# Optimization experiments

Hardware: AMD Instinct MI355X
Metric: run time of the kernel (lower is better)

Reference implementation:

```python
import jax, jax.numpy as jnp
from jax import lax
import numpy as np

GWS = (2, 7, 7)          # grid_window_size
NUM_HEADS = 4
DIM = 256
HEAD_DIM = DIM // NUM_HEADS
SCALE = HEAD_DIM ** -0.5


def _rel_index(ws):
    d, h, w = ws
    coords = np.stack(np.meshgrid(np.arange(d), np.arange(h), np.arange(w), indexing='ij')).reshape(3, -1)
    rel = (coords[:, :, None] - coords[:, None, :]).transpose(1, 2, 0)
    rel[:, :, 0] += d - 1
    rel[:, :, 1] += h - 1
    rel[:, :, 2] += w - 1
    rel[:, :, 0] *= (2 * h - 1) * (2 * w - 1)
    rel[:, :, 1] *= (2 * w - 1)
    return rel.sum(-1)

RPI = jnp.asarray(_rel_index(GWS))  # (98, 98) int, constant buffer


def _ln(x, w, b, eps=1e-5):
    m = x.mean(-1, keepdims=True)
    v = ((x - m) ** 2).mean(-1, keepdims=True)
    return (x - m) * lax.rsqrt(v + eps) * w + b


def _attention(x, qkv_w, proj_w, proj_b, bias_table):
    # x: (num_windows, N, C); qkv has no bias in the original (qkv_bias=False)
    Bw, N, C = x.shape
    qkv = (x @ qkv_w.T).reshape(Bw, N, 3, NUM_HEADS, HEAD_DIM).transpose(2, 0, 3, 1, 4)
    q, k, v = qkv[0] * SCALE, qkv[1], qkv[2]
    scores = jnp.einsum('bhnd,bhmd->bhnm', q, k)
    bias = bias_table[RPI.reshape(-1)].reshape(N, N, NUM_HEADS).transpose(2, 0, 1)
    a = jax.nn.softmax(scores + bias[None], axis=-1)
    out = jnp.einsum('bhnm,bhmd->bhnd', a, v).transpose(0, 2, 1, 3).reshape(Bw, N, C)
    return out @ proj_w.T + proj_b


def _window_partition(x):
    B, D, H, W, C = x.shape
    d, h, w = GWS
    x = x.reshape(B, D // d, d, H // h, h, W // w, w, C).transpose(0, 1, 3, 5, 2, 4, 6, 7)
    return x.reshape(-1, d * h * w, C)


def _window_reverse(win, B, D, H, W):
    d, h, w = GWS
    x = win.reshape(B, D // d, H // h, W // w, d, h, w, -1).transpose(0, 1, 4, 2, 5, 3, 6, 7)
    return x.reshape(B, D, H, W, -1)


def _grid_partition(x):
    B, D, H, W, C = x.shape
    d, h, w = GWS
    x = x.reshape(B, d, D // d, h, H // h, w, W // w, C).transpose(0, 2, 4, 6, 1, 3, 5, 7)
    return x.reshape(-1, d * h * w, C)


def _grid_reverse(g, B, D, H, W):
    d, h, w = GWS
    x = g.reshape(B, D // d, H // h, W // w, d, h, w, -1).transpose(0, 4, 1, 5, 2, 6, 3, 7)
    return x.reshape(B, D, H, W, -1)


def _conv3d(x, w, b):
    y = lax.conv_general_dilated(x, w, (1, 1, 1), 'SAME',
                                 dimension_numbers=('NCDHW', 'OIDHW', 'NCDHW'))
    return y + b[None, :, None, None, None]


def _leaky(x):
    return jnp.where(x >= 0, x, 0.01 * x)


def setup_inputs() -> dict:
    key = jax.random.key(0)
    ks = jax.random.split(key, 12)
    B, D, H, W = 2, 8, 56, 56
    dim = DIM
    TBL = (2 * GWS[0] - 1) * (2 * GWS[1] - 1) * (2 * GWS[2] - 1)  # 507
    p = lambda k, s: jax.random.normal(k, s, jnp.float32) * 0.02
    return {
        'input': jax.random.normal(ks[0], (B, dim, D, H, W), jnp.float32),
        'n1w': jnp.ones((dim,), jnp.float32), 'n1b': jnp.zeros((dim,), jnp.float32),
        'n2w': jnp.ones((dim,), jnp.float32), 'n2b': jnp.zeros((dim,), jnp.float32),
        'wqkv': p(ks[1], (3 * dim, dim)),
        'wprojw': p(ks[2], (dim, dim)), 'wprojb': jnp.zeros((dim,), jnp.float32),
        'wbias': p(ks[3], (TBL, NUM_HEADS)),
        'gqkv': p(ks[4], (3 * dim, dim)),
        'gprojw': p(ks[5], (dim, dim)), 'gprojb': jnp.zeros((dim,), jnp.float32),
        'gbias': p(ks[6], (TBL, NUM_HEADS)),
        'f1c1w': p(ks[7], (128, 128, 3, 3, 3)), 'f1c1b': jnp.zeros((128,), jnp.float32),
        'f1c2w': p(ks[8], (128, 128, 3, 3, 3)), 'f1c2b': jnp.zeros((128,), jnp.float32),
        'g1c1w': p(ks[9], (128, 128, 3, 3, 3)), 'g1c1b': jnp.zeros((128,), jnp.float32),
        'g1c2w': p(ks[10], (128, 128, 3, 3, 3)), 'g1c2b': jnp.zeros((128,), jnp.float32),
    }


def reference(input, n1w, n1b, n2w, n2b, wqkv, wprojw, wprojb, wbias,
              gqkv, gprojw, gprojb, gbias,
              f1c1w, f1c1b, f1c2w, f1c2b, g1c1w, g1c1b, g1c2w, g1c2b):
    B, C, D, H, W = input.shape
    x = input.transpose(0, 2, 3, 4, 1)  # b d h w c
    x = _ln(x, n1w, n1b)
    pd = (GWS[0] - D % GWS[0]) % GWS[0]
    ph = (GWS[1] - H % GWS[1]) % GWS[1]
    pw = (GWS[2] - W % GWS[2]) % GWS[2]
    if pd or ph or pw:
        x = jnp.pad(x, ((0, 0), (0, pd), (0, ph), (0, pw), (0, 0)))
    Dp, Hp, Wp = D + pd, H + ph, W + pw
    # block (window) attention
    win = _window_partition(x)
    win = _attention(win, wqkv, wprojw, wprojb, wbias)
    xw = _window_reverse(win, B, Dp, Hp, Wp)
    # grid attention
    y = _ln(xw, n2w, n2b)
    g = _grid_partition(y)
    g = _attention(g, gqkv, gprojw, gprojb, gbias)
    y = _grid_reverse(g, B, Dp, Hp, Wp) + xw
    if pd or ph or pw:
        y = y[:, :D, :H, :W, :]
    y = y.transpose(0, 4, 1, 2, 3)  # b c d h w
    s = input + y
    # reversible conv block: split 256 -> 128/128
    x1, x2 = s[:, :C // 2], s[:, C // 2:]
    y1 = x1 + _conv3d(_leaky(_conv3d(x2, f1c1w, f1c1b)), f1c2w, f1c2b)
    y2 = x2 + _conv3d(_leaky(_conv3d(y1, g1c1w, g1c1b)), g1c2w, g1c2b)
    return jnp.concatenate([y1, y2], axis=1)
```

## Files before the change

### kernel.cpp

```cpp
#include <hip/hip_runtime.h>
#include <stdint.h>


typedef unsigned short u16;
typedef __attribute__((ext_vector_type(8))) short short8;
typedef __attribute__((ext_vector_type(4))) float f32x4;

#define TOK   50176
#define CH    256
#define SPAT  25088
#define PLANE 3136

__device__ __forceinline__ float b2f(u16 u) {
    union { uint32_t i; float f; } v; v.i = ((uint32_t)u) << 16; return v.f;
}
__device__ __forceinline__ u16 f2b(float f) {
    union { float f; uint32_t i; } v; v.f = f;
    uint32_t i = v.i;
    uint32_t r = i + 0x7FFFu + ((i >> 16) & 1u);
    return (u16)(r >> 16);
}

__global__ __launch_bounds__(256) void ln1_kernel(
    const float* __restrict__ x, const float* __restrict__ w,
    const float* __restrict__ bsh, u16* __restrict__ out)
{
    int t = blockIdx.x * 256 + threadIdx.x;
    int b = t / SPAT, sp = t % SPAT;
    const float* px = x + (size_t)b * CH * SPAT + sp;
    float s = 0.f, ss = 0.f;
    for (int c = 0; c < CH; c++) { float v = px[(size_t)c * SPAT]; s += v; ss += v * v; }
    float mean = s * (1.0f / CH);
    float var  = ss * (1.0f / CH) - mean * mean;
    float rstd = rsqrtf(var + 1e-5f);
    u16* po = out + (size_t)t * CH;
    for (int c = 0; c < CH; c++) {
        float v = (px[(size_t)c * SPAT] - mean) * rstd * w[c] + bsh[c];
        po[c] = f2b(v);
    }
}

__global__ __launch_bounds__(256) void ln2_kernel(
    const u16* __restrict__ x, const float* __restrict__ w,
    const float* __restrict__ bsh, u16* __restrict__ out)
{
    int wave = threadIdx.x >> 6, lane = threadIdx.x & 63;
    int t = blockIdx.x * 4 + wave;
    const u16* px = x + (size_t)t * CH + lane * 4;
    ushort4 v4 = *(const ushort4*)px;
    float v0 = b2f(v4.x), v1 = b2f(v4.y), v2 = b2f(v4.z), v3 = b2f(v4.w);
    float s = v0 + v1 + v2 + v3;
    float ss = v0*v0 + v1*v1 + v2*v2 + v3*v3;
    for (int o = 32; o > 0; o >>= 1) {
        s  += __shfl_xor(s,  o, 64);
        ss += __shfl_xor(ss, o, 64);
    }
    float mean = s * (1.0f / CH);
    float rstd = rsqrtf(ss * (1.0f / CH) - mean * mean + 1e-5f);
    float4 w4 = *(const float4*)(w + lane * 4);
    float4 b4 = *(const float4*)(bsh + lane * 4);
    ushort4 o4;
    o4.x = f2b((v0 - mean) * rstd * w4.x + b4.x);
    o4.y = f2b((v1 - mean) * rstd * w4.y + b4.y);
    o4.z = f2b((v2 - mean) * rstd * w4.z + b4.z);
    o4.w = f2b((v3 - mean) * rstd * w4.w + b4.w);
    *(ushort4*)(out + (size_t)t * CH + lane * 4) = o4;
}

__global__ __launch_bounds__(256) void gemm_mfma_kernel(
    const u16* __restrict__ A, const float* __restrict__ B,
    const float* __restrict__ bias, const u16* __restrict__ res,
    u16* __restrict__ C, int Nout)
{
    __shared__ u16 sAg[128][72];
    __shared__ u16 sBg[128][72];
    int tid = threadIdx.x;
    int m0 = blockIdx.x * 128, n0g = blockIdx.y * 128;
    int lane = tid & 63, wv = tid >> 6;
    int quad = lane >> 4, l15 = lane & 15;
    int mw = (wv & 1) * 64, nw = (wv >> 1) * 64;

    f32x4 zz = {0.f, 0.f, 0.f, 0.f};
    f32x4 acc[4][4];
    #pragma unroll
    for (int i = 0; i < 4; i++)
        #pragma unroll
        for (int j = 0; j < 4; j++) acc[i][j] = zz;

    for (int kc = 0; kc < 256; kc += 64) {
        __syncthreads();
        #pragma unroll
        for (int i = 0; i < 4; i++) {
            int unit = tid + i * 256;
            int row = unit >> 3, k8 = (unit & 7) << 3;
            *(uint4*)&sAg[row][k8] = *(const uint4*)(A + (size_t)(m0 + row) * 256 + kc + k8);
        }
        #pragma unroll
        for (int i = 0; i < 8; i++) {
            int unit = tid + i * 256;
            int row = unit >> 4, k4 = (unit & 15) << 2;
            float4 v = *(const float4*)(B + (size_t)(n0g + row) * 256 + kc + k4);
            ushort4 p;
            p.x = f2b(v.x); p.y = f2b(v.y); p.z = f2b(v.z); p.w = f2b(v.w);
            *(ushort4*)&sBg[row][k4] = p;
        }
        __syncthreads();
        #pragma unroll
        for (int kk = 0; kk < 2; kk++) {
            short8 afr[4], bfr[4];
            #pragma unroll
            for (int mt = 0; mt < 4; mt++)
                afr[mt] = *(const short8*)&sAg[mw + mt*16 + l15][kk*32 + quad*8];
            #pragma unroll
            for (int nt = 0; nt < 4; nt++)
                bfr[nt] = *(const short8*)&sBg[nw + nt*16 + l15][kk*32 + quad*8];
            #pragma unroll
            for (int mt = 0; mt < 4; mt++)
                #pragma unroll
                for (int nt = 0; nt < 4; nt++)
                    acc[mt][nt] = __builtin_amdgcn_mfma_f32_16x16x32_bf16(
                        afr[mt], bfr[nt], acc[mt][nt], 0, 0, 0);
        }
    }

    #pragma unroll
    for (int nt = 0; nt < 4; nt++) {
        int n = n0g + nw + nt*16 + l15;
        float bv = bias ? bias[n] : 0.f;
        #pragma unroll
        for (int mt = 0; mt < 4; mt++) {
            int m = m0 + mw + mt*16 + quad*4;
            #pragma unroll
            for (int r = 0; r < 4; r++) {
                float v = acc[mt][nt][r] + bv;
                size_t off = (size_t)(m + r) * Nout + n;
                if (res) v += b2f(res[off]);
                C[off] = f2b(v);
            }
        }
    }
}

__global__ __launch_bounds__(256) void attn_mfma_kernel(
    const u16* __restrict__ qkv, const float* __restrict__ btab,
    u16* __restrict__ outp, int mode)
{
    __shared__ u16 sKV[8704];
    __shared__ u16 sS[112][136];
    __shared__ float sBias[507];
    __shared__ int sTok[112];
    __shared__ int sEnc[112];
    __shared__ float sInv[112];

    int g = blockIdx.x, head = blockIdx.y, tid = threadIdx.x;
    int b  = g >> 8;
    int gd = (g >> 6) & 3, gh = (g >> 3) & 7, gw = g & 7;

    int lane = tid & 63, wv = tid >> 6;
    int quad = lane >> 4, l15 = lane & 15;
    int mts[2] = {wv, wv + 4};

    if (tid < 112) {
        int t = tid;
        int i = t / 49, r = t % 49, j = r / 7, k = r % 7;
        sEnc[tid] = i * 169 + j * 13 + k;
        int tokv = 0;
        if (t < 98) {
            int d, h, w;
            if (mode == 0) { d = gd*2 + i; h = gh*7 + j; w = gw*7 + k; }
            else           { d = i*4 + gd; h = j*8 + gh; w = k*8 + gw; }
            tokv = ((b*8 + d)*56 + h)*56 + w;
        }
        sTok[tid] = tokv;
    }
    for (int idx = tid; idx < 507; idx += 256) sBias[idx] = btab[idx * 4 + head];
    __syncthreads();

    for (int idx = tid; idx < 112 * 8; idx += 256) {
        int row = idx >> 3, c8 = (idx & 7) << 3;
        uint4 v = {0u, 0u, 0u, 0u};
        if (row < 98)
            v = *(const uint4*)(qkv + (size_t)sTok[row] * 768 + 256 + head * 64 + c8);
        *(uint4*)&sKV[row * 72 + c8] = v;
    }
    __syncthreads();

    short8 qf[2][2];
    #pragma unroll
    for (int mi = 0; mi < 2; mi++) {
        int mt = mts[mi];
        #pragma unroll
        for (int ks = 0; ks < 2; ks++) {
            short8 v;
            #pragma unroll
            for (int j = 0; j < 8; j++) v[j] = 0;
            int row = mt * 16 + l15;
            if (mt < 7 && row < 98)
                v = *(const short8*)(qkv + (size_t)sTok[row] * 768 + head * 64 + ks * 32 + quad * 8);
            qf[mi][ks] = v;
        }
    }

    f32x4 zz = {0.f, 0.f, 0.f, 0.f};
    #pragma unroll
    for (int mi = 0; mi < 2; mi++) {
        int mt = mts[mi];
        if (mt >= 7) continue;
        for (int nt = 0; nt < 7; nt++) {
            f32x4 acc = zz;
            acc = __builtin_amdgcn_mfma_f32_16x16x32_bf16(
                qf[mi][0], *(const short8*)&sKV[(nt*16 + l15) * 72 + quad*8], acc, 0, 0, 0);
            acc = __builtin_amdgcn_mfma_f32_16x16x32_bf16(
                qf[mi][1], *(const short8*)&sKV[(nt*16 + l15) * 72 + 32 + quad*8], acc, 0, 0, 0);
            int n = nt * 16 + l15;
            int en = (n < 98) ? sEnc[n] : 0;
            #pragma unroll
            for (int r = 0; r < 4; r++) {
                int m = mt * 16 + quad * 4 + r;
                float v;
                if (n < 98) {
                    int em = sEnc[m < 98 ? m : 97];
                    v = acc[r] * 0.125f + sBias[em - en + 253];
                } else v = -1e30f;
                sS[m][n] = f2b(v);
            }
        }
    }
    __syncthreads();

    for (int idx = tid; idx < 64 * 30; idx += 256) {
        int c = idx / 30, t = 98 + idx % 30;
        sKV[c * 136 + t] = 0;
    }
    for (int idx = tid; idx < 98 * 8; idx += 256) {
        int tok = idx >> 3, c8 = (idx & 7) << 3;
        uint4 v = *(const uint4*)(qkv + (size_t)sTok[tok] * 768 + 512 + head * 64 + c8);
        const u16* pv = (const u16*)&v;
        #pragma unroll
        for (int j = 0; j < 8; j++) sKV[(c8 + j) * 136 + tok] = pv[j];
    }

    {
        int row = tid >> 1, half = tid & 1;
        if (row < 112) {
            #pragma unroll
            for (int j = 0; j < 8; j++) sS[row][112 + half * 8 + j] = 0;
        }
        if (row < 98) {
            int c0 = half * 49;
            float mx = -1e30f;
            for (int j = 0; j < 49; j++) mx = fmaxf(mx, b2f(sS[row][c0 + j]));
            mx = fmaxf(mx, __shfl_xor(mx, 1, 64));
            float sum = 0.f;
            for (int j = 0; j < 49; j++) {
                float e = __expf(b2f(sS[row][c0 + j]) - mx);
                sum += e;
                sS[row][c0 + j] = f2b(e);
            }
            sum += __shfl_xor(sum, 1, 64);
            if (half == 0) sInv[row] = 1.0f / sum;
        }
    }
    __syncthreads();

    f32x4 po[2][4];
    #pragma unroll
    for (int mi = 0; mi < 2; mi++)
        #pragma unroll
        for (int nt = 0; nt < 4; nt++) po[mi][nt] = zz;

    #pragma unroll
    for (int mi = 0; mi < 2; mi++) {
        int mt = mts[mi];
        if (mt >= 7) continue;
        for (int ks = 0; ks < 4; ks++) {
            short8 ap = *(const short8*)&sS[mt*16 + l15][ks*32 + quad*8];
            #pragma unroll
            for (int nt = 0; nt < 4; nt++) {
                short8 bv = *(const short8*)&sKV[(nt*16 + l15) * 136 + ks*32 + quad*8];
                po[mi][nt] = __builtin_amdgcn_mfma_f32_16x16x32_bf16(ap, bv, po[mi][nt], 0, 0, 0);
            }
        }
    }

    #pragma unroll
    for (int mi = 0; mi < 2; mi++) {
        int mt = mts[mi];
        if (mt >= 7) continue;
        #pragma unroll
        for (int r = 0; r < 4; r++) {
            int m = mt * 16 + quad * 4 + r;
            if (m >= 98) continue;
            float inv = sInv[m];
            u16* dst = outp + (size_t)sTok[m] * 256 + head * 64 + l15;
            #pragma unroll
            for (int nt = 0; nt < 4; nt++)
                dst[nt * 16] = f2b(po[mi][nt][r] * inv);
        }
    }
}

__global__ __launch_bounds__(256) void ssplit_cl_kernel(
    const float* __restrict__ inp, const u16* __restrict__ y,
    u16* __restrict__ s1, u16* __restrict__ s2)
{
    __shared__ float sT[64][65];
    int t0 = blockIdx.x * 64;
    int b = t0 / SPAT, sp0 = t0 % SPAT;
    int tid = threadIdx.x;
    for (int cg = 0; cg < 4; cg++) {
        __syncthreads();
        #pragma unroll
        for (int i = 0; i < 16; i++) {
            int unit = tid + i * 256;
            int cl = unit >> 6, spl = unit & 63;
            sT[spl][cl] = inp[((size_t)(b * 256 + cg * 64 + cl)) * SPAT + sp0 + spl];
        }
        __syncthreads();
        int spl = tid >> 2, c16 = (tid & 3) * 16;
        int tok = t0 + spl;
        const u16* yp = y + (size_t)tok * 256 + cg * 64 + c16;
        int cbase = cg * 64 + c16;
        u16* dst = (cbase < 128) ? (s1 + (size_t)tok * 128 + cbase)
                                 : (s2 + (size_t)tok * 128 + cbase - 128);
        #pragma unroll
        for (int j = 0; j < 16; j++) {
            float v = sT[spl][c16 + j] + b2f(yp[j]);
            dst[j] = f2b(v);
        }
    }
}

__global__ __launch_bounds__(256) void convw_kernel(
    const float* __restrict__ w, u16* __restrict__ o)
{
    int e = blockIdx.x * 256 + threadIdx.x;
    int k = e >> 14;
    int r = e & 16383;
    o[e] = f2b(w[(size_t)r * 27 + k]);
}

__global__ __launch_bounds__(256) void conv_mfma_kernel(
    const u16* __restrict__ in_cl,
    const u16* __restrict__ wt27,
    const float* __restrict__ bias,
    const u16* __restrict__ res_cl,
    u16* __restrict__ out_cl,
    float* __restrict__ out_f32,
    int oc_base, int leaky)
{
    __shared__ u16 sA[64][136];
    __shared__ u16 sB[128][136];
    __shared__ int sD[64], sHH[64], sWW[64];

    int tid = threadIdx.x;
    int t0 = blockIdx.x * 64;
    int b = t0 / SPAT, sp0 = t0 % SPAT;

    if (tid < 64) {
        int sp = sp0 + tid;
        int d = sp / PLANE, r = sp % PLANE;
        sD[tid] = d; sHH[tid] = r / 56; sWW[tid] = r % 56;
    }

    int lane = tid & 63, wv = tid >> 6;
    int quad = lane >> 4, l15 = lane & 15;
    int n0 = wv * 32;

    f32x4 zz = {0.f, 0.f, 0.f, 0.f};
    f32x4 acc[4][2];
    #pragma unroll
    for (int i = 0; i < 4; i++) { acc[i][0] = zz; acc[i][1] = zz; }

    __syncthreads();

    for (int ko = 0; ko < 27; ko++) {
        int kd = ko / 9 - 1, kh = (ko / 3) % 3 - 1, kw = ko % 3 - 1;
        __syncthreads();
        #pragma unroll
        for (int i = 0; i < 4; i++) {
            int unit = tid + i * 256;
            int m = unit >> 4, k8 = (unit & 15) << 3;
            int dd = sD[m] + kd, hh = sHH[m] + kh, ww = sWW[m] + kw;
            uint4 v = {0u, 0u, 0u, 0u};
            if ((unsigned)dd < 8u && (unsigned)hh < 56u && (unsigned)ww < 56u) {
                size_t sp = (size_t)(b * 8 + dd) * PLANE + hh * 56 + ww;
                v = *(const uint4*)(in_cl + sp * 128 + k8);
            }
            *(uint4*)&sA[m][k8] = v;
        }
        const u16* wp = wt27 + (size_t)ko * 16384;
        #pragma unroll
        for (int i = 0; i < 8; i++) {
            int unit = tid + i * 256;
            int oc = unit >> 4, k8 = (unit & 15) << 3;
            *(uint4*)&sB[oc][k8] = *(const uint4*)(wp + oc * 128 + k8);
        }
        __syncthreads();
        #pragma unroll
        for (int kk = 0; kk < 4; kk++) {
            short8 afr[4], bfr[2];
            #pragma unroll
            for (int mt = 0; mt < 4; mt++)
                afr[mt] = *(const short8*)&sA[mt*16 + l15][kk*32 + quad*8];
            #pragma unroll
            for (int nt = 0; nt < 2; nt++)
                bfr[nt] = *(const short8*)&sB[n0 + nt*16 + l15][kk*32 + quad*8];
            #pragma unroll
            for (int mt = 0; mt < 4; mt++)
                #pragma unroll
                for (int nt = 0; nt < 2; nt++)
                    acc[mt][nt] = __builtin_amdgcn_mfma_f32_16x16x32_bf16(
                        afr[mt], bfr[nt], acc[mt][nt], 0, 0, 0);
        }
    }

    #pragma unroll
    for (int nt = 0; nt < 2; nt++) {
        int oc = n0 + nt*16 + l15;
        float bv = bias[oc];
        #pragma unroll
        for (int mt = 0; mt < 4; mt++) {
            int m = mt*16 + quad*4;
            #pragma unroll
            for (int r = 0; r < 4; r++) {
                float v = acc[mt][nt][r] + bv;
                if (leaky) v = (v >= 0.f) ? v : 0.01f * v;
                if (res_cl) v += b2f(res_cl[(size_t)(t0 + m + r) * 128 + oc]);
                acc[mt][nt][r] = v;
            }
        }
    }

    if (out_cl) {
        #pragma unroll
        for (int mt = 0; mt < 4; mt++) {
            int m = mt*16 + quad*4;
            #pragma unroll
            for (int nt = 0; nt < 2; nt++) {
                int oc = n0 + nt*16 + l15;
                #pragma unroll
                for (int r = 0; r < 4; r++)
                    out_cl[(size_t)(t0 + m + r) * 128 + oc] = f2b(acc[mt][nt][r]);
            }
        }
    }

    if (out_f32) {
        __syncthreads();
        float* sT = (float*)&sB[0][0];
        #pragma unroll
        for (int mt = 0; mt < 4; mt++) {
            int m = mt*16 + quad*4;
            #pragma unroll
            for (int nt = 0; nt < 2; nt++) {
                int oc = n0 + nt*16 + l15;
                #pragma unroll
                for (int r = 0; r < 4; r++)
                    sT[oc * 65 + m + r] = acc[mt][nt][r];
            }
        }
        __syncthreads();
        int oc = tid >> 1, half = tid & 1;
        size_t obase = ((size_t)b * 256 + oc_base + oc) * SPAT + sp0 + half * 32;
        const float* row = &sT[oc * 65 + half * 32];
        for (int j = 0; j < 32; j++) out_f32[obase + j] = row[j];
    }
}

extern "C" void kernel_launch(void* const* d_in, const int* in_sizes, int n_in,
                              void* d_out, int out_size, void* d_ws, size_t ws_size,
                              hipStream_t stream)
{
    const float* input  = (const float*)d_in[0];
    const float* n1w    = (const float*)d_in[1];
    const float* n1b    = (const float*)d_in[2];
    const float* n2w    = (const float*)d_in[3];
    const float* n2b    = (const float*)d_in[4];
    const float* wqkv   = (const float*)d_in[5];
    const float* wprojw = (const float*)d_in[6];
    const float* wprojb = (const float*)d_in[7];
    const float* wbias  = (const float*)d_in[8];
    const float* gqkv   = (const float*)d_in[9];
    const float* gprojw = (const float*)d_in[10];
    const float* gprojb = (const float*)d_in[11];
    const float* gbias  = (const float*)d_in[12];
    const float* f1c1w  = (const float*)d_in[13];
    const float* f1c1b  = (const float*)d_in[14];
    const float* f1c2w  = (const float*)d_in[15];
    const float* f1c2b  = (const float*)d_in[16];
    const float* g1c1w  = (const float*)d_in[17];
    const float* g1c1b  = (const float*)d_in[18];
    const float* g1c2w  = (const float*)d_in[19];
    const float* g1c2b  = (const float*)d_in[20];

    char* ws = (char*)d_ws;
    u16* xln   = (u16*)(ws);
    u16* qkv   = (u16*)(ws + 25690112);
    u16* attnb = (u16*)(ws + 102760448);
    u16* xw    = (u16*)(ws + 128450560);
    u16* y  = xln;
    u16* s1   = qkv;
    u16* s2   = (u16*)(ws + 25690112 + 12845056);
    u16* tb   = (u16*)(ws + 25690112 + 25690112);
    u16* y1cl = (u16*)(ws + 25690112 + 38535168);
    u16* cw0  = (u16*)(ws + 25690112 + 51380224);
    u16* cw1  = cw0 + 442368;
    u16* cw2  = cw1 + 442368;
    u16* cw3  = cw2 + 442368;

    float* outp = (float*)d_out;

    ln1_kernel<<<196, 256, 0, stream>>>(input, n1w, n1b, xln);
    gemm_mfma_kernel<<<dim3(392, 6), 256, 0, stream>>>(xln, wqkv, nullptr, nullptr, qkv, 768);
    attn_mfma_kernel<<<dim3(512, 4), 256, 0, stream>>>(qkv, wbias, attnb, 0);
    gemm_mfma_kernel<<<dim3(392, 2), 256, 0, stream>>>(attnb, wprojw, wprojb, nullptr, xw, 256);
    ln2_kernel<<<12544, 256, 0, stream>>>(xw, n2w, n2b, xln);
    gemm_mfma_kernel<<<dim3(392, 6), 256, 0, stream>>>(xln, gqkv, nullptr, nullptr, qkv, 768);
    attn_mfma_kernel<<<dim3(512, 4), 256, 0, stream>>>(qkv, gbias, attnb, 1);
    gemm_mfma_kernel<<<dim3(392, 2), 256, 0, stream>>>(attnb, gprojw, gprojb, xw, y, 256);
    ssplit_cl_kernel<<<784, 256, 0, stream>>>(input, y, s1, s2);
    convw_kernel<<<1728, 256, 0, stream>>>(f1c1w, cw0);
    convw_kernel<<<1728, 256, 0, stream>>>(f1c2w, cw1);
    convw_kernel<<<1728, 256, 0, stream>>>(g1c1w, cw2);
    convw_kernel<<<1728, 256, 0, stream>>>(g1c2w, cw3);
    conv_mfma_kernel<<<784, 256, 0, stream>>>(s2, cw0, f1c1b, nullptr, tb, nullptr, 0, 1);
    conv_mfma_kernel<<<784, 256, 0, stream>>>(tb, cw1, f1c2b, s1, y1cl, outp, 0, 0);
    conv_mfma_kernel<<<784, 256, 0, stream>>>(y1cl, cw2, g1c1b, nullptr, tb, nullptr, 0, 1);
    conv_mfma_kernel<<<784, 256, 0, stream>>>(tb, cw3, g1c2b, s2, nullptr, outp, 128, 0);
}
```

Baseline: 961.8 us.

## Load conv MFMA fragments directly from global memory, drop LDS staging

The 3D conv kernel stops staging input and weight tiles through shared memory each of its 27 taps, so the per-tap barriers go away. Each wave now loads its A and B MFMA fragments straight from global memory, relying on cache reuse. Blocks shrink to 128 threads (2 waves), each computing a 64-output-channel slice with a 4x4 accumulator tile. LDS is allocated dynamically only for the fp32 transpose store, which now writes float4 values. The risk is redundant global and L2 traffic, because there is no longer explicit on-chip reuse of weights across waves, and the larger accumulator tile raises register pressure.

```diff
diff --git a/kernel.cpp b/kernel.cpp
--- a/kernel.cpp
+++ b/kernel.cpp
@@ -340,7 +340,8 @@
     o[e] = f2b(w[(size_t)r * 27 + k]);
 }
 
-__global__ __launch_bounds__(256) void conv_mfma_kernel(
+extern __shared__ float conv_smem[];
+__global__ __launch_bounds__(128, 3) void conv_mfma_kernel(
     const u16* __restrict__ in_cl,
     const u16* __restrict__ wt27,
     const float* __restrict__ bias,
@@ -349,75 +350,70 @@
     float* __restrict__ out_f32,
     int oc_base, int leaky)
 {
-    __shared__ u16 sA[64][136];
-    __shared__ u16 sB[128][136];
-    __shared__ int sD[64], sHH[64], sWW[64];
-
     int tid = threadIdx.x;
     int t0 = blockIdx.x * 64;
     int b = t0 / SPAT, sp0 = t0 % SPAT;
-
-    if (tid < 64) {
-        int sp = sp0 + tid;
-        int d = sp / PLANE, r = sp % PLANE;
-        sD[tid] = d; sHH[tid] = r / 56; sWW[tid] = r % 56;
-    }
-
     int lane = tid & 63, wv = tid >> 6;
     int quad = lane >> 4, l15 = lane & 15;
-    int n0 = wv * 32;
+    int nw = wv * 64;
+
+    int dm[4], hm[4], wm[4];
+    const u16* abase[4];
+    #pragma unroll
+    for (int mt = 0; mt < 4; mt++) {
+        int sp = sp0 + mt*16 + l15;
+        dm[mt] = sp / PLANE;
+        int r = sp % PLANE;
+        hm[mt] = r / 56; wm[mt] = r % 56;
+        abase[mt] = in_cl + ((size_t)b * SPAT + sp) * 128 + quad * 8;
+    }
+    int boff[4];
+    #pragma unroll
+    for (int nt = 0; nt < 4; nt++)
+        boff[nt] = (nw + nt*16 + l15) * 128 + quad * 8;
 
     f32x4 zz = {0.f, 0.f, 0.f, 0.f};
-    f32x4 acc[4][2];
-    #pragma unroll
-    for (int i = 0; i < 4; i++) { acc[i][0] = zz; acc[i][1] = zz; }
-
-    __syncthreads();
+    f32x4 acc[4][4];
+    #pragma unroll
+    for (int i = 0; i < 4; i++)
+        #pragma unroll
+        for (int j = 0; j < 4; j++) acc[i][j] = zz;
+
+    short8 z8;
+    #pragma unroll
+    for (int j = 0; j < 8; j++) z8[j] = 0;
 
     for (int ko = 0; ko < 27; ko++) {
         int kd = ko / 9 - 1, kh = (ko / 3) % 3 - 1, kw = ko % 3 - 1;
-        __syncthreads();
-        #pragma unroll
-        for (int i = 0; i < 4; i++) {
-            int unit = tid + i * 256;
-            int m = unit >> 4, k8 = (unit & 15) << 3;
-            int dd = sD[m] + kd, hh = sHH[m] + kh, ww = sWW[m] + kw;
-            uint4 v = {0u, 0u, 0u, 0u};
-            if ((unsigned)dd < 8u && (unsigned)hh < 56u && (unsigned)ww < 56u) {
-                size_t sp = (size_t)(b * 8 + dd) * PLANE + hh * 56 + ww;
-                v = *(const uint4*)(in_cl + sp * 128 + k8);
-            }
-            *(uint4*)&sA[m][k8] = v;
-        }
-        const u16* wp = wt27 + (size_t)ko * 16384;
-        #pragma unroll
-        for (int i = 0; i < 8; i++) {
-            int unit = tid + i * 256;
-            int oc = unit >> 4, k8 = (unit & 15) << 3;
-            *(uint4*)&sB[oc][k8] = *(const uint4*)(wp + oc * 128 + k8);
-        }
-        __syncthreads();
+        int soff = (kd * PLANE + kh * 56 + kw) * 128;
+        const u16* wbase = wt27 + ko * 16384;
+        bool val[4];
+        #pragma unroll
+        for (int mt = 0; mt < 4; mt++)
+            val[mt] = (unsigned)(dm[mt] + kd) < 8u &&
+                      (unsigned)(hm[mt] + kh) < 56u &&
+                      (unsigned)(wm[mt] + kw) < 56u;
         #pragma unroll
         for (int kk = 0; kk < 4; kk++) {
-            short8 afr[4], bfr[2];
+            short8 afr[4], bfr[4];
             #pragma unroll
             for (int mt = 0; mt < 4; mt++)
-                afr[mt] = *(const short8*)&sA[mt*16 + l15][kk*32 + quad*8];
-            #pragma unroll
-            for (int nt = 0; nt < 2; nt++)
-                bfr[nt] = *(const short8*)&sB[n0 + nt*16 + l15][kk*32 + quad*8];
+                afr[mt] = val[mt] ? *(const short8*)(abase[mt] + soff + kk*32) : z8;
+            #pragma unroll
+            for (int nt = 0; nt < 4; nt++)
+                bfr[nt] = *(const short8*)(wbase + boff[nt] + kk*32);
             #pragma unroll
             for (int mt = 0; mt < 4; mt++)
                 #pragma unroll
-                for (int nt = 0; nt < 2; nt++)
+                for (int nt = 0; nt < 4; nt++)
                     acc[mt][nt] = __builtin_amdgcn_mfma_f32_16x16x32_bf16(
                         afr[mt], bfr[nt], acc[mt][nt], 0, 0, 0);
         }
     }
 
     #pragma unroll
-    for (int nt = 0; nt < 2; nt++) {
-        int oc = n0 + nt*16 + l15;
+    for (int nt = 0; nt < 4; nt++) {
+        int oc = nw + nt*16 + l15;
         float bv = bias[oc];
         #pragma unroll
         for (int mt = 0; mt < 4; mt++) {
@@ -437,8 +433,8 @@
         for (int mt = 0; mt < 4; mt++) {
             int m = mt*16 + quad*4;
             #pragma unroll
-            for (int nt = 0; nt < 2; nt++) {
-                int oc = n0 + nt*16 + l15;
+            for (int nt = 0; nt < 4; nt++) {
+                int oc = nw + nt*16 + l15;
                 #pragma unroll
                 for (int r = 0; r < 4; r++)
                     out_cl[(size_t)(t0 + m + r) * 128 + oc] = f2b(acc[mt][nt][r]);
@@ -447,24 +443,27 @@
     }
 
     if (out_f32) {
-        __syncthreads();
-        float* sT = (float*)&sB[0][0];
+        float* sT = conv_smem;
         #pragma unroll
         for (int mt = 0; mt < 4; mt++) {
             int m = mt*16 + quad*4;
             #pragma unroll
-            for (int nt = 0; nt < 2; nt++) {
-                int oc = n0 + nt*16 + l15;
+            for (int nt = 0; nt < 4; nt++) {
+                int oc = nw + nt*16 + l15;
                 #pragma unroll
                 for (int r = 0; r < 4; r++)
-                    sT[oc * 65 + m + r] = acc[mt][nt][r];
+                    sT[oc * 67 + m + r] = acc[mt][nt][r];
             }
         }
         __syncthreads();
-        int oc = tid >> 1, half = tid & 1;
-        size_t obase = ((size_t)b * 256 + oc_base + oc) * SPAT + sp0 + half * 32;
-        const float* row = &sT[oc * 65 + half * 32];
-        for (int j = 0; j < 32; j++) out_f32[obase + j] = row[j];
+        int oc = tid;
+        float* dst = out_f32 + ((size_t)b * 256 + oc_base + oc) * SPAT + sp0;
+        const float* row = &sT[oc * 67];
+        #pragma unroll
+        for (int j = 0; j < 16; j++) {
+            float4 v = { row[j*4+0], row[j*4+1], row[j*4+2], row[j*4+3] };
+            *(float4*)(dst + j*4) = v;
+        }
     }
 }
 
@@ -510,6 +509,7 @@
     u16* cw3  = cw2 + 442368;
 
     float* outp = (float*)d_out;
+    const int F32_LDS = 128 * 67 * 4;
 
     ln1_kernel<<<196, 256, 0, stream>>>(input, n1w, n1b, xln);
     gemm_mfma_kernel<<<dim3(392, 6), 256, 0, stream>>>(xln, wqkv, nullptr, nullptr, qkv, 768);
@@ -524,8 +524,8 @@
     convw_kernel<<<1728, 256, 0, stream>>>(f1c2w, cw1);
     convw_kernel<<<1728, 256, 0, stream>>>(g1c1w, cw2);
     convw_kernel<<<1728, 256, 0, stream>>>(g1c2w, cw3);
-    conv_mfma_kernel<<<784, 256, 0, stream>>>(s2, cw0, f1c1b, nullptr, tb, nullptr, 0, 1);
-    conv_mfma_kernel<<<784, 256, 0, stream>>>(tb, cw1, f1c2b, s1, y1cl, outp, 0, 0);
-    conv_mfma_kernel<<<784, 256, 0, stream>>>(y1cl, cw2, g1c1b, nullptr, tb, nullptr, 0, 1);
-    conv_mfma_kernel<<<784, 256, 0, stream>>>(tb, cw3, g1c2b, s2, nullptr, outp, 128, 0);
-}
+    conv_mfma_kernel<<<784, 128, 0, stream>>>(s2, cw0, f1c1b, nullptr, tb, nullptr, 0, 1);
+    conv_mfma_kernel<<<784, 128, F32_LDS, stream>>>(tb, cw1, f1c2b, s1, y1cl, outp, 0, 0);
+    conv_mfma_kernel<<<784, 128, 0, stream>>>(y1cl, cw2, g1c1b, nullptr, tb, nullptr, 0, 1);
+    conv_mfma_kernel<<<784, 128, F32_LDS, stream>>>(tb, cw3, g1c2b, s2, nullptr, outp, 128, 0);
+}
```

After: 1.252 ms. 30.2% more time.

## Double-buffer conv input tiles and read pre-swizzled weights directly from global

Applied to the files above, without the earlier changes.

Reorders the conv weights on the host-side prep kernel into MFMA fragment order, so each wave loads B fragments straight from global or L2 instead of staging 128x128 weights in LDS every tap. The input tile is stored in LDS in fragment-contiguous layout and double-buffered, with the next tap's global loads issued into registers before the current MFMAs. This cuts it to one barrier per tap and frees LDS to allow 3 blocks per CU via launch bounds. The fp32 transpose buffer also moves to an XOR-style rotation in a 64-wide layout. The risk is that weight fragments are re-read from global by every block, and register pressure rises from the prefetch buffers.

```diff
diff --git a/kernel.cpp b/kernel.cpp
--- a/kernel.cpp
+++ b/kernel.cpp
@@ -335,22 +335,28 @@
     const float* __restrict__ w, u16* __restrict__ o)
 {
     int e = blockIdx.x * 256 + threadIdx.x;
-    int k = e >> 14;
+    int tap = e >> 14;
     int r = e & 16383;
-    o[e] = f2b(w[(size_t)r * 27 + k]);
-}
-
-__global__ __launch_bounds__(256) void conv_mfma_kernel(
+    int kk = r >> 12;
+    int nt = (r >> 9) & 7;
+    int quad = (r >> 7) & 3;
+    int l15 = (r >> 3) & 15;
+    int j = r & 7;
+    int oc = nt * 16 + l15;
+    int ic = kk * 32 + quad * 8 + j;
+    o[e] = f2b(w[(size_t)(oc * 128 + ic) * 27 + tap]);
+}
+
+__global__ __launch_bounds__(256, 3) void conv_mfma_kernel(
     const u16* __restrict__ in_cl,
-    const u16* __restrict__ wt27,
+    const u16* __restrict__ wtf,
     const float* __restrict__ bias,
     const u16* __restrict__ res_cl,
     u16* __restrict__ out_cl,
     float* __restrict__ out_f32,
     int oc_base, int leaky)
 {
-    __shared__ u16 sA[64][136];
-    __shared__ u16 sB[128][136];
+    __shared__ u16 sA[2][8192];
     __shared__ int sD[64], sHH[64], sWW[64];
 
     int tid = threadIdx.x;
@@ -362,50 +368,64 @@
         int d = sp / PLANE, r = sp % PLANE;
         sD[tid] = d; sHH[tid] = r / 56; sWW[tid] = r % 56;
     }
+    __syncthreads();
 
     int lane = tid & 63, wv = tid >> 6;
     int quad = lane >> 4, l15 = lane & 15;
     int n0 = wv * 32;
 
+    int u_l15[4], u_kq[4], u_m[4];
+    #pragma unroll
+    for (int i = 0; i < 4; i++) {
+        int unit = tid + i * 256;
+        int mtkk = unit >> 6;
+        int mt = mtkk & 3;
+        u_m[i]  = mt * 16 + (unit & 15);
+        u_kq[i] = ((mtkk >> 2) * 32 + ((unit >> 4) & 3) * 8);
+        u_l15[i] = unit;
+    }
+
     f32x4 zz = {0.f, 0.f, 0.f, 0.f};
     f32x4 acc[4][2];
     #pragma unroll
     for (int i = 0; i < 4; i++) { acc[i][0] = zz; acc[i][1] = zz; }
 
+    uint4 pre[4];
+
+    #define STAGE_REGS(TAP)                                                    \
+    {                                                                          \
+        int kd = (TAP) / 9 - 1, kh = ((TAP) / 3) % 3 - 1, kw = (TAP) % 3 - 1;  \
+        _Pragma("unroll")                                                      \
+        for (int i = 0; i < 4; i++) {                                          \
+            int m = u_m[i];                                                    \
+            int dd = sD[m] + kd, hh = sHH[m] + kh, ww = sWW[m] + kw;           \
+            uint4 v = {0u, 0u, 0u, 0u};                                        \
+            if ((unsigned)dd < 8u && (unsigned)hh < 56u && (unsigned)ww < 56u) \
+                v = *(const uint4*)(in_cl +                                    \
+                    ((size_t)(b * 8 + dd) * PLANE + hh * 56 + ww) * 128 + u_kq[i]); \
+            pre[i] = v;                                                        \
+        }                                                                      \
+    }
+
+    STAGE_REGS(0);
+    #pragma unroll
+    for (int i = 0; i < 4; i++) *(uint4*)&sA[0][u_l15[i] * 8] = pre[i];
     __syncthreads();
 
-    for (int ko = 0; ko < 27; ko++) {
-        int kd = ko / 9 - 1, kh = (ko / 3) % 3 - 1, kw = ko % 3 - 1;
-        __syncthreads();
-        #pragma unroll
-        for (int i = 0; i < 4; i++) {
-            int unit = tid + i * 256;
-            int m = unit >> 4, k8 = (unit & 15) << 3;
-            int dd = sD[m] + kd, hh = sHH[m] + kh, ww = sWW[m] + kw;
-            uint4 v = {0u, 0u, 0u, 0u};
-            if ((unsigned)dd < 8u && (unsigned)hh < 56u && (unsigned)ww < 56u) {
-                size_t sp = (size_t)(b * 8 + dd) * PLANE + hh * 56 + ww;
-                v = *(const uint4*)(in_cl + sp * 128 + k8);
-            }
-            *(uint4*)&sA[m][k8] = v;
-        }
-        const u16* wp = wt27 + (size_t)ko * 16384;
-        #pragma unroll
-        for (int i = 0; i < 8; i++) {
-            int unit = tid + i * 256;
-            int oc = unit >> 4, k8 = (unit & 15) << 3;
-            *(uint4*)&sB[oc][k8] = *(const uint4*)(wp + oc * 128 + k8);
-        }
-        __syncthreads();
+    for (int tap = 0; tap < 27; tap++) {
+        int cur = tap & 1;
+        if (tap < 26) STAGE_REGS(tap + 1);
+
+        const u16* wb = wtf + tap * 16384;
         #pragma unroll
         for (int kk = 0; kk < 4; kk++) {
             short8 afr[4], bfr[2];
             #pragma unroll
             for (int mt = 0; mt < 4; mt++)
-                afr[mt] = *(const short8*)&sA[mt*16 + l15][kk*32 + quad*8];
+                afr[mt] = *(const short8*)&sA[cur][((kk*4 + mt)*64 + lane) * 8];
             #pragma unroll
             for (int nt = 0; nt < 2; nt++)
-                bfr[nt] = *(const short8*)&sB[n0 + nt*16 + l15][kk*32 + quad*8];
+                bfr[nt] = *(const short8*)(wb + ((kk*8 + n0/16 + nt)*64 + lane) * 8);
             #pragma unroll
             for (int mt = 0; mt < 4; mt++)
                 #pragma unroll
@@ -413,7 +433,14 @@
                     acc[mt][nt] = __builtin_amdgcn_mfma_f32_16x16x32_bf16(
                         afr[mt], bfr[nt], acc[mt][nt], 0, 0, 0);
         }
-    }
+
+        if (tap < 26) {
+            #pragma unroll
+            for (int i = 0; i < 4; i++) *(uint4*)&sA[cur ^ 1][u_l15[i] * 8] = pre[i];
+        }
+        __syncthreads();
+    }
+    #undef STAGE_REGS
 
     #pragma unroll
     for (int nt = 0; nt < 2; nt++) {
@@ -448,7 +475,7 @@
 
     if (out_f32) {
         __syncthreads();
-        float* sT = (float*)&sB[0][0];
+        float* sT = (float*)&sA[0][0];
         #pragma unroll
         for (int mt = 0; mt < 4; mt++) {
             int m = mt*16 + quad*4;
@@ -457,14 +484,17 @@
                 int oc = n0 + nt*16 + l15;
                 #pragma unroll
                 for (int r = 0; r < 4; r++)
-                    sT[oc * 65 + m + r] = acc[mt][nt][r];
+                    sT[oc * 64 + ((m + r + oc) & 63)] = acc[mt][nt][r];
             }
         }
         __syncthreads();
         int oc = tid >> 1, half = tid & 1;
         size_t obase = ((size_t)b * 256 + oc_base + oc) * SPAT + sp0 + half * 32;
-        const float* row = &sT[oc * 65 + half * 32];
-        for (int j = 0; j < 32; j++) out_f32[obase + j] = row[j];
+        const float* row = &sT[oc * 64];
+        for (int j = 0; j < 32; j++) {
+            int m = half * 32 + j;
+            out_f32[obase + j] = row[(m + oc) & 63];
+        }
     }
 }
 
```

After: 854.1 us. 1.13x faster.
